# Kernel tuning notes

Hardware: AMD Instinct MI355X
Metric: run time of the kernel (lower is better)

## Reference

```python
import jax, jax.numpy as jnp
import numpy as np
import math

T = 4096        # block_size / sequence length
E = 2048        # embedding_dim
D = 256         # head_dim


def setup_inputs() -> dict:
    key = jax.random.key(0)
    k_x, k_q, k_k, k_v = jax.random.split(key, 4)
    x = jax.random.normal(k_x, (T, E), dtype=jnp.float32)
    # nn.Linear weights are [out_features, in_features]
    s = 1.0 / math.sqrt(E)
    Wq = jax.random.normal(k_q, (D, E), dtype=jnp.float32) * s
    Wk = jax.random.normal(k_k, (D, E), dtype=jnp.float32) * s
    Wv = jax.random.normal(k_v, (D, E), dtype=jnp.float32) * s
    return {"x": x, "Wq": Wq, "Wk": Wk, "Wv": Wv}


def reference(x, Wq, Wk, Wv):
    # Projections: x @ W.T  (torch Linear, no bias)
    Q = x @ Wq.T            # [T, D]
    K = x @ Wk.T            # [T, D]
    V = x @ Wv.T            # [T, D]
    scale = 1.0 / math.sqrt(Q.shape[-1])
    scores = (Q @ K.T) * scale                      # [T, T]
    causal = jnp.tril(jnp.ones((T, T), dtype=bool))
    scores = jnp.where(causal, scores, jnp.float32(-1e10))
    probs = jax.nn.softmax(scores, axis=-1)         # row softmax (torch legacy dim=1 for 2-D)
    return probs @ V                                # [T, D]
```

## Files before the change

### kernel.cpp

```cpp
#include <hip/hip_runtime.h>
#include <hip/hip_bf16.h>

#define T_DIM 4096
#define E_DIM 2048
#define D_DIM 256

typedef __attribute__((ext_vector_type(4))) float f32x4;
typedef __attribute__((ext_vector_type(8))) short s16x8;

__device__ __forceinline__ unsigned short f2bf(float f) {
  unsigned int u = __float_as_uint(f);
  unsigned int r = (u + 0x7FFFu + ((u >> 16) & 1u)) >> 16;
  return (unsigned short)r;
}
__device__ __forceinline__ float bf2f(unsigned short h) {
  return __uint_as_float(((unsigned int)h) << 16);
}

__device__ __forceinline__ f32x4 mfma16(s16x8 a, s16x8 b, f32x4 c) {
  return __builtin_amdgcn_mfma_f32_16x16x32_bf16(a, b, c, 0, 0, 0);
}

__device__ __forceinline__ void gload_lds16(const void* g, void* l) {
  __builtin_amdgcn_global_load_lds((const __attribute__((address_space(1))) void*)g,
                                   (__attribute__((address_space(3))) void*)l, 16, 0, 0);
}

__global__ __launch_bounds__(256) void cvt_all(const float* __restrict__ x,
                                               const float* __restrict__ wq,
                                               const float* __restrict__ wk,
                                               const float* __restrict__ wv,
                                               unsigned short* __restrict__ xb,
                                               unsigned short* __restrict__ wb) {
  int blk = blockIdx.x;
  const float* src;
  unsigned short* dst;
  int rel;
  if (blk < 4096)      { src = x;  dst = xb;           rel = blk; }
  else if (blk < 4352) { src = wq; dst = wb;           rel = blk - 4096; }
  else if (blk < 4608) { src = wk; dst = wb + 524288;  rel = blk - 4352; }
  else                 { src = wv; dst = wb + 1048576; rel = blk - 4608; }
  int i = rel * 256 + threadIdx.x;
  float4 a = ((const float4*)src)[i * 2];
  float4 b = ((const float4*)src)[i * 2 + 1];
  uint4 o;
  o.x = (unsigned int)f2bf(a.x) | ((unsigned int)f2bf(a.y) << 16);
  o.y = (unsigned int)f2bf(a.z) | ((unsigned int)f2bf(a.w) << 16);
  o.z = (unsigned int)f2bf(b.x) | ((unsigned int)f2bf(b.y) << 16);
  o.w = (unsigned int)f2bf(b.z) | ((unsigned int)f2bf(b.w) << 16);
  ((uint4*)dst)[i] = o;
}

__global__ __launch_bounds__(256, 3) void qkv_gemm(
    const unsigned short* __restrict__ xb, const unsigned short* __restrict__ wb,
    unsigned short* __restrict__ Qg, unsigned short* __restrict__ Kg,
    unsigned short* __restrict__ Vt) {
  __shared__ __align__(16) unsigned short Al[2][128 * 64];
  __shared__ __align__(16) unsigned short Bl[2][64 * 64];
  int tid = threadIdx.x, wid = tid >> 6, lane = tid & 63;
  int lr = lane & 15, lk = lane >> 4;
  int bi_ = (int)blockIdx.x;
  int xcd = bi_ & 7, kk = bi_ >> 3;
  int mb_ = (kk / 12) * 8 + xcd, nb_ = kk % 12;
  int bm0 = mb_ * 128, bn0 = nb_ * 64;
  int wm = (wid >> 1) * 64, wn = (wid & 1) * 32;

  f32x4 acc[4][2];
#pragma unroll
  for (int m = 0; m < 4; ++m)
#pragma unroll
    for (int n = 0; n < 2; ++n) acc[m][n] = (f32x4){0.f, 0.f, 0.f, 0.f};

#define STAGE_QKV(kt, buf)                                                              \
  {                                                                                     \
    int k0 = (kt)*64;                                                                   \
    _Pragma("unroll") for (int i2 = 0; i2 < 4; ++i2) {                                  \
      int ci = (wid * 4 + i2) * 64 + lane;                                              \
      int row = ci >> 3, cc = ci & 7;                                                   \
      gload_lds16(&xb[(size_t)(bm0 + row) * E_DIM + k0 + ((cc ^ (row & 7)) << 3)],      \
                  &Al[buf][(size_t)(wid * 4 + i2) * 512]);                              \
    }                                                                                   \
    _Pragma("unroll") for (int i2 = 0; i2 < 2; ++i2) {                                  \
      int ci = (wid * 2 + i2) * 64 + lane;                                              \
      int row = ci >> 3, cc = ci & 7;                                                   \
      gload_lds16(&wb[(size_t)(bn0 + row) * E_DIM + k0 + ((cc ^ (row & 7)) << 3)],      \
                  &Bl[buf][(size_t)(wid * 2 + i2) * 512]);                              \
    }                                                                                   \
  }

  STAGE_QKV(0, 0);
  for (int kt = 0; kt < 32; ++kt) {
    int cur = kt & 1;
    __builtin_amdgcn_s_barrier();
    if (kt + 1 < 32) {
      STAGE_QKV(kt + 1, cur ^ 1);
      asm volatile("s_waitcnt vmcnt(6)" ::: "memory");
    } else {
      asm volatile("s_waitcnt vmcnt(0)" ::: "memory");
    }
    __builtin_amdgcn_s_barrier();
    s16x8 af[2][4], bfr[2][2];
#pragma unroll
    for (int c = 0; c < 2; ++c) {
#pragma unroll
      for (int m = 0; m < 4; ++m)
        af[c][m] = *(const s16x8*)&Al[cur][(size_t)(wm + m * 16 + lr) * 64 +
                                           (((c * 4 + lk) ^ (lr & 7)) << 3)];
#pragma unroll
      for (int n = 0; n < 2; ++n)
        bfr[c][n] = *(const s16x8*)&Bl[cur][(size_t)(wn + n * 16 + lr) * 64 +
                                            (((c * 4 + lk) ^ (lr & 7)) << 3)];
    }
#pragma unroll
    for (int c = 0; c < 2; ++c)
#pragma unroll
      for (int m = 0; m < 4; ++m)
#pragma unroll
        for (int n = 0; n < 2; ++n) acc[m][n] = mfma16(af[c][m], bfr[c][n], acc[m][n]);
  }

#pragma unroll
  for (int m = 0; m < 4; ++m) {
    int grow = bm0 + wm + m * 16 + lk * 4;
#pragma unroll
    for (int n = 0; n < 2; ++n) {
      int gcol = bn0 + wn + n * 16 + lr;
      unsigned short h[4];
#pragma unroll
      for (int r = 0; r < 4; ++r) h[r] = f2bf(acc[m][n][r]);
      if (gcol < 256) {
#pragma unroll
        for (int r = 0; r < 4; ++r) Qg[(size_t)(grow + r) * D_DIM + gcol] = h[r];
      } else if (gcol < 512) {
#pragma unroll
        for (int r = 0; r < 4; ++r) Kg[(size_t)(grow + r) * D_DIM + gcol - 256] = h[r];
      } else {
        uint2 w;
        w.x = (unsigned int)h[0] | ((unsigned int)h[1] << 16);
        w.y = (unsigned int)h[2] | ((unsigned int)h[3] << 16);
        *(uint2*)&Vt[(size_t)(gcol - 512) * T_DIM + grow] = w;
      }
    }
  }
#undef STAGE_QKV
}

__global__ __launch_bounds__(512, 2) void attn_kernel(
    const unsigned short* __restrict__ Qg, const unsigned short* __restrict__ Kg,
    const unsigned short* __restrict__ Vt, unsigned short* __restrict__ Opart,
    float* __restrict__ mpart, float* __restrict__ lpart) {
  __shared__ __align__(16) unsigned short Kl[2][64 * 256];
  __shared__ __align__(16) unsigned short Vl[2][256 * 64];
  __shared__ __align__(16) unsigned short Pl[8][16 * 64];

  int bi = (int)blockIdx.x;
  int j = (bi & 7) * 66 + (bi >> 3);
  int t = (int)((sqrtf(8.0f * (float)j + 1.0f) - 1.0f) * 0.5f);
  while (t > 0 && t * (t + 1) / 2 > j) --t;
  while ((t + 1) * (t + 2) / 2 <= j) ++t;
  int s = j - t * (t + 1) / 2;

  int tid = threadIdx.x, wid = tid >> 6, lane = tid & 63;
  int lr = lane & 15, lk = lane >> 4;
  int q0w = t * 128 + wid * 16;
  unsigned short* pl = &Pl[wid][0];

#define STAGE_KV(jt, buf)                                                            \
  {                                                                                  \
    int kv_ = (jt)*64;                                                               \
    _Pragma("unroll") for (int i2 = 0; i2 < 4; ++i2) {                               \
      int idx = (wid * 4 + i2) * 64 + lane;                                          \
      int row = idx >> 5, g = idx & 31;                                              \
      gload_lds16(&Kg[(size_t)(kv_ + row) * D_DIM + ((g ^ (row & 7)) << 3)],         \
                  &Kl[buf][(size_t)(wid * 4 + i2) * 512]);                           \
    }                                                                                \
    _Pragma("unroll") for (int i2 = 0; i2 < 4; ++i2) {                               \
      int idx = (wid * 4 + i2) * 64 + lane;                                          \
      int d_ = idx >> 3, g = idx & 7;                                                \
      gload_lds16(&Vt[(size_t)d_ * T_DIM + kv_ + ((g ^ (d_ & 7)) << 3)],             \
                  &Vl[buf][(size_t)(wid * 4 + i2) * 512]);                           \
    }                                                                                \
  }

  STAGE_KV(2 * s, 0);

  s16x8 qf[8];
#pragma unroll
  for (int c = 0; c < 8; ++c)
    qf[c] = *(const s16x8*)&Qg[(size_t)(q0w + lr) * D_DIM + c * 32 + lk * 8];

  float m_run = -1e30f, l_run = 0.f;
  f32x4 Oa[16];
#pragma unroll
  for (int d = 0; d < 16; ++d) Oa[d] = (f32x4){0.f, 0.f, 0.f, 0.f};
  const float scale = 0.0625f;
  int sw = lr & 7;

#pragma unroll
  for (int n = 0; n < 2; ++n) {
    int jt = 2 * s + n, kv = jt * 64, cur = n;
    __builtin_amdgcn_s_barrier();
    if (n == 0) {
      STAGE_KV(jt + 1, 1);
      asm volatile("s_waitcnt vmcnt(8)" ::: "memory");
    } else {
      asm volatile("s_waitcnt vmcnt(0)" ::: "memory");
    }
    __builtin_amdgcn_s_barrier();
    const unsigned short* kl = &Kl[cur][0];
    const unsigned short* vl = &Vl[cur][0];

    f32x4 sa[4];
#pragma unroll
    for (int jb = 0; jb < 4; ++jb) sa[jb] = (f32x4){0.f, 0.f, 0.f, 0.f};
#pragma unroll
    for (int jb = 0; jb < 4; ++jb) {
      int rowbase = (jb * 16 + lr) * 256;
#pragma unroll
      for (int c = 0; c < 8; ++c) {
        s16x8 kf = *(const s16x8*)&kl[(size_t)rowbase + (((c * 4 + lk) ^ sw) << 3)];
        sa[jb] = mfma16(kf, qf[c], sa[jb]);
      }
    }

    bool needmask = (kv + 63 > q0w);
    int myq = q0w + lr;
    float tmax = -1e30f;
#pragma unroll
    for (int jb = 0; jb < 4; ++jb) {
#pragma unroll
      for (int r = 0; r < 4; ++r) {
        float v = sa[jb][r] * scale;
        if (needmask && (kv + jb * 16 + lk * 4 + r) > myq) v = -1e30f;
        sa[jb][r] = v;
        tmax = fmaxf(tmax, v);
      }
    }
    tmax = fmaxf(tmax, __shfl_xor(tmax, 16));
    tmax = fmaxf(tmax, __shfl_xor(tmax, 32));
    float m_new = fmaxf(fmaxf(m_run, tmax), -1e29f);
    float alpha = __expf(m_run - m_new);
    float psum = 0.f;
#pragma unroll
    for (int jb = 0; jb < 4; ++jb) {
      float p0 = __expf(sa[jb][0] - m_new);
      float p1 = __expf(sa[jb][1] - m_new);
      float p2 = __expf(sa[jb][2] - m_new);
      float p3 = __expf(sa[jb][3] - m_new);
      psum += (p0 + p1) + (p2 + p3);
      uint2 w;
      w.x = (unsigned int)f2bf(p0) | ((unsigned int)f2bf(p1) << 16);
      w.y = (unsigned int)f2bf(p2) | ((unsigned int)f2bf(p3) << 16);
      *(uint2*)&pl[(size_t)lr * 64 + (((jb * 2 + (lk >> 1)) ^ sw) << 3) + (lk & 1) * 4] = w;
    }
    psum += __shfl_xor(psum, 16);
    psum += __shfl_xor(psum, 32);
    l_run = l_run * alpha + psum;
    m_run = m_new;

    float al[4];
#pragma unroll
    for (int r = 0; r < 4; ++r) al[r] = __shfl(alpha, lk * 4 + r);
#pragma unroll
    for (int d = 0; d < 16; ++d) {
#pragma unroll
      for (int r = 0; r < 4; ++r) Oa[d][r] *= al[r];
    }

    s16x8 pf[2];
#pragma unroll
    for (int ks = 0; ks < 2; ++ks)
      pf[ks] = *(const s16x8*)&pl[(size_t)lr * 64 + (((ks * 4 + lk) ^ sw) << 3)];
#pragma unroll
    for (int d = 0; d < 16; ++d) {
#pragma unroll
      for (int ks = 0; ks < 2; ++ks) {
        s16x8 vf = *(const s16x8*)&vl[(size_t)(d * 16 + lr) * 64 +
                                      (((ks * 4 + lk) ^ sw) << 3)];
        Oa[d] = mfma16(pf[ks], vf, Oa[d]);
      }
    }
  }

#pragma unroll
  for (int d = 0; d < 16; ++d) {
    unsigned short h[4];
#pragma unroll
    for (int r = 0; r < 4; ++r) h[r] = f2bf(Oa[d][r]);
    uint2 w;
    w.x = (unsigned int)h[0] | ((unsigned int)h[1] << 16);
    w.y = (unsigned int)h[2] | ((unsigned int)h[3] << 16);
    *(uint2*)&Opart[((size_t)j * 256 + d * 16 + lr) * 128 + wid * 16 + lk * 4] = w;
  }
  if (lk == 0) {
    mpart[(size_t)j * 128 + wid * 16 + lr] = m_run;
    lpart[(size_t)j * 128 + wid * 16 + lr] = l_run;
  }
#undef STAGE_KV
}

__global__ __launch_bounds__(256) void merge_kernel(const unsigned short* __restrict__ Opart,
                                                    const float* __restrict__ mpart,
                                                    const float* __restrict__ lpart,
                                                    float* __restrict__ out) {
  __shared__ float trans[128 * 33];
  int blk = blockIdx.x;
  int t = blk >> 3, d0 = (blk & 7) * 32, q0 = t * 128;
  int ql = threadIdx.x & 127, dg = threadIdx.x >> 7;
  int base = t * (t + 1) / 2, np = t + 1;

  float M = -1e30f, den = 0.f;
  float acc[16];
#pragma unroll
  for (int k = 0; k < 16; ++k) acc[k] = 0.f;

#pragma unroll 1
  for (int p = 0; p < np; ++p) {
    float mp = mpart[(size_t)(base + p) * 128 + ql];
    float lp = lpart[(size_t)(base + p) * 128 + ql];
    float Mn = fmaxf(M, mp);
    float sc = __expf(M - Mn);
    float w = __expf(mp - Mn);
    den = den * sc + w * lp;
    const unsigned short* op = &Opart[((size_t)(base + p) * 256 + d0 + dg) * 128 + ql];
#pragma unroll
    for (int k = 0; k < 16; ++k) acc[k] = acc[k] * sc + w * bf2f(op[(size_t)(2 * k) * 128]);
    M = Mn;
  }
  float inv = 1.0f / den;
#pragma unroll
  for (int k = 0; k < 16; ++k) trans[ql * 33 + dg + 2 * k] = acc[k] * inv;
  __syncthreads();

#pragma unroll
  for (int k = 0; k < 16; ++k) {
    int q = (threadIdx.x >> 5) + 8 * k;
    int dd = threadIdx.x & 31;
    out[(size_t)(q0 + q) * 256 + d0 + dd] = trans[q * 33 + dd];
  }
}

extern "C" void kernel_launch(void* const* d_in, const int* in_sizes, int n_in,
                              void* d_out, int out_size, void* d_ws, size_t ws_size,
                              hipStream_t stream) {
  const float* x  = (const float*)d_in[0];
  const float* Wq = (const float*)d_in[1];
  const float* Wk = (const float*)d_in[2];
  const float* Wv = (const float*)d_in[3];

  char* ws = (char*)d_ws;
  unsigned short* xb = (unsigned short*)(ws);
  unsigned short* wb = (unsigned short*)(ws + 16777216);
  unsigned short* Qg = (unsigned short*)(ws + 19922944);
  unsigned short* Kg = (unsigned short*)(ws + 22020096);
  unsigned short* Vt = (unsigned short*)(ws + 24117248);
  unsigned short* Opart = (unsigned short*)(ws + 26214400);
  float* mpart = (float*)(ws + 60817408);
  float* lpart = (float*)(ws + 61087744);

  cvt_all<<<4864, 256, 0, stream>>>(x, Wq, Wk, Wv, xb, wb);
  qkv_gemm<<<384, 256, 0, stream>>>(xb, wb, Qg, Kg, Vt);
  attn_kernel<<<528, 512, 0, stream>>>(Qg, Kg, Vt, Opart, mpart, lpart);
  merge_kernel<<<256, 256, 0, stream>>>(Opart, mpart, lpart, (float*)d_out);
}
```

Measured before the change: 97.90 us.

## Halve KV tile to 32 rows to raise attention occupancy, add setprio around MFMA

The attention kernel now streams K/V in 32-row tiles instead of 64. This halves LDS use so launch bounds can request 4 blocks per CU instead of 2. The loop becomes a rolled 4-iteration double-buffered pipeline with a new swizzle for the narrower V and P tiles, and s_setprio raises wave priority around the MFMA sections. The aim is better latency hiding through more resident waves. The cost is more barriers and softmax rescale steps per tile, and possible register spills under the tighter launch bound.

```diff
diff --git a/kernel.cpp b/kernel.cpp
--- a/kernel.cpp
+++ b/kernel.cpp
@@ -145,13 +145,13 @@
 #undef STAGE_QKV
 }
 
-__global__ __launch_bounds__(512, 2) void attn_kernel(
+__global__ __launch_bounds__(512, 4) void attn_kernel(
     const unsigned short* __restrict__ Qg, const unsigned short* __restrict__ Kg,
     const unsigned short* __restrict__ Vt, unsigned short* __restrict__ Opart,
     float* __restrict__ mpart, float* __restrict__ lpart) {
-  __shared__ __align__(16) unsigned short Kl[2][64 * 256];
-  __shared__ __align__(16) unsigned short Vl[2][256 * 64];
-  __shared__ __align__(16) unsigned short Pl[8][16 * 64];
+  __shared__ __align__(16) unsigned short Kl[2][32 * 256];
+  __shared__ __align__(16) unsigned short Vl[2][256 * 32];
+  __shared__ __align__(16) unsigned short Pl[8][16 * 32];
 
   int bi = (int)blockIdx.x;
   int j = (bi & 7) * 66 + (bi >> 3);
@@ -167,22 +167,22 @@
 
 #define STAGE_KV(jt, buf)                                                            \
   {                                                                                  \
-    int kv_ = (jt)*64;                                                               \
-    _Pragma("unroll") for (int i2 = 0; i2 < 4; ++i2) {                               \
-      int idx = (wid * 4 + i2) * 64 + lane;                                          \
+    int kv_ = (jt)*32;                                                               \
+    _Pragma("unroll") for (int i2 = 0; i2 < 2; ++i2) {                               \
+      int idx = (wid * 2 + i2) * 64 + lane;                                          \
       int row = idx >> 5, g = idx & 31;                                              \
       gload_lds16(&Kg[(size_t)(kv_ + row) * D_DIM + ((g ^ (row & 7)) << 3)],         \
-                  &Kl[buf][(size_t)(wid * 4 + i2) * 512]);                           \
+                  &Kl[buf][(size_t)(wid * 2 + i2) * 512]);                           \
     }                                                                                \
-    _Pragma("unroll") for (int i2 = 0; i2 < 4; ++i2) {                               \
-      int idx = (wid * 4 + i2) * 64 + lane;                                          \
-      int d_ = idx >> 3, g = idx & 7;                                                \
-      gload_lds16(&Vt[(size_t)d_ * T_DIM + kv_ + ((g ^ (d_ & 7)) << 3)],             \
-                  &Vl[buf][(size_t)(wid * 4 + i2) * 512]);                           \
+    _Pragma("unroll") for (int i2 = 0; i2 < 2; ++i2) {                               \
+      int idx = (wid * 2 + i2) * 64 + lane;                                          \
+      int d_ = idx >> 2, g = idx & 3;                                                \
+      gload_lds16(&Vt[(size_t)d_ * T_DIM + kv_ + ((g ^ ((d_ >> 1) & 3)) << 3)],      \
+                  &Vl[buf][(size_t)(wid * 2 + i2) * 512]);                           \
     }                                                                                \
   }
 
-  STAGE_KV(2 * s, 0);
+  STAGE_KV(4 * s, 0);
 
   s16x8 qf[8];
 #pragma unroll
@@ -195,14 +195,15 @@
   for (int d = 0; d < 16; ++d) Oa[d] = (f32x4){0.f, 0.f, 0.f, 0.f};
   const float scale = 0.0625f;
   int sw = lr & 7;
-
-#pragma unroll
-  for (int n = 0; n < 2; ++n) {
-    int jt = 2 * s + n, kv = jt * 64, cur = n;
+  int sw2 = (lr >> 1) & 3;
+
+#pragma unroll 1
+  for (int n = 0; n < 4; ++n) {
+    int jt = 4 * s + n, kv = jt * 32, cur = n & 1;
     __builtin_amdgcn_s_barrier();
-    if (n == 0) {
-      STAGE_KV(jt + 1, 1);
-      asm volatile("s_waitcnt vmcnt(8)" ::: "memory");
+    if (n < 3) {
+      STAGE_KV(jt + 1, cur ^ 1);
+      asm volatile("s_waitcnt vmcnt(4)" ::: "memory");
     } else {
       asm volatile("s_waitcnt vmcnt(0)" ::: "memory");
     }
@@ -210,11 +211,12 @@
     const unsigned short* kl = &Kl[cur][0];
     const unsigned short* vl = &Vl[cur][0];
 
-    f32x4 sa[4];
-#pragma unroll
-    for (int jb = 0; jb < 4; ++jb) sa[jb] = (f32x4){0.f, 0.f, 0.f, 0.f};
-#pragma unroll
-    for (int jb = 0; jb < 4; ++jb) {
+    f32x4 sa[2];
+    sa[0] = (f32x4){0.f, 0.f, 0.f, 0.f};
+    sa[1] = (f32x4){0.f, 0.f, 0.f, 0.f};
+    __builtin_amdgcn_s_setprio(1);
+#pragma unroll
+    for (int jb = 0; jb < 2; ++jb) {
       int rowbase = (jb * 16 + lr) * 256;
 #pragma unroll
       for (int c = 0; c < 8; ++c) {
@@ -222,12 +224,13 @@
         sa[jb] = mfma16(kf, qf[c], sa[jb]);
       }
     }
-
-    bool needmask = (kv + 63 > q0w);
+    __builtin_amdgcn_s_setprio(0);
+
+    bool needmask = (kv + 31 > q0w);
     int myq = q0w + lr;
     float tmax = -1e30f;
 #pragma unroll
-    for (int jb = 0; jb < 4; ++jb) {
+    for (int jb = 0; jb < 2; ++jb) {
 #pragma unroll
       for (int r = 0; r < 4; ++r) {
         float v = sa[jb][r] * scale;
@@ -242,7 +245,7 @@
     float alpha = __expf(m_run - m_new);
     float psum = 0.f;
 #pragma unroll
-    for (int jb = 0; jb < 4; ++jb) {
+    for (int jb = 0; jb < 2; ++jb) {
       float p0 = __expf(sa[jb][0] - m_new);
       float p1 = __expf(sa[jb][1] - m_new);
       float p2 = __expf(sa[jb][2] - m_new);
@@ -251,7 +254,7 @@
       uint2 w;
       w.x = (unsigned int)f2bf(p0) | ((unsigned int)f2bf(p1) << 16);
       w.y = (unsigned int)f2bf(p2) | ((unsigned int)f2bf(p3) << 16);
-      *(uint2*)&pl[(size_t)lr * 64 + (((jb * 2 + (lk >> 1)) ^ sw) << 3) + (lk & 1) * 4] = w;
+      *(uint2*)&pl[(size_t)lr * 32 + (((jb * 2 + (lk >> 1)) ^ sw2) << 3) + (lk & 1) * 4] = w;
     }
     psum += __shfl_xor(psum, 16);
     psum += __shfl_xor(psum, 32);
@@ -267,19 +270,14 @@
       for (int r = 0; r < 4; ++r) Oa[d][r] *= al[r];
     }
 
-    s16x8 pf[2];
-#pragma unroll
-    for (int ks = 0; ks < 2; ++ks)
-      pf[ks] = *(const s16x8*)&pl[(size_t)lr * 64 + (((ks * 4 + lk) ^ sw) << 3)];
+    s16x8 pf = *(const s16x8*)&pl[(size_t)lr * 32 + ((lk ^ sw2) << 3)];
+    __builtin_amdgcn_s_setprio(1);
 #pragma unroll
     for (int d = 0; d < 16; ++d) {
-#pragma unroll
-      for (int ks = 0; ks < 2; ++ks) {
-        s16x8 vf = *(const s16x8*)&vl[(size_t)(d * 16 + lr) * 64 +
-                                      (((ks * 4 + lk) ^ sw) << 3)];
-        Oa[d] = mfma16(pf[ks], vf, Oa[d]);
-      }
-    }
+      s16x8 vf = *(const s16x8*)&vl[(size_t)(d * 16 + lr) * 32 + ((lk ^ sw2) << 3)];
+      Oa[d] = mfma16(pf, vf, Oa[d]);
+    }
+    __builtin_amdgcn_s_setprio(0);
   }
 
 #pragma unroll
```

Measured after the change: 131.7 us. 34.5% more time.
